# Optimization experiments

Hardware: AMD Instinct MI355X
Metric: run time of the kernel (lower is better)

## Reference

```python
import jax, jax.numpy as jnp
import numpy as np

H = 16  # n_heads

def setup_inputs() -> dict:
    key = jax.random.key(0)
    ks = jax.random.split(key, 11)
    B, L, D = 2, 2048, 1024
    w = 1.0 / np.sqrt(D).astype(np.float32)
    return {
        "query": jax.random.normal(ks[0], (B, L, D), jnp.float32),
        "key":   jax.random.normal(ks[1], (B, L, D), jnp.float32),
        "value": jax.random.normal(ks[2], (B, L, D), jnp.float32),
        "Wq": jax.random.normal(ks[3], (D, D), jnp.float32) * w,
        "bq": jax.random.normal(ks[4], (D,), jnp.float32) * 0.01,
        "Wk": jax.random.normal(ks[5], (D, D), jnp.float32) * w,
        "bk": jax.random.normal(ks[6], (D,), jnp.float32) * 0.01,
        "Wv": jax.random.normal(ks[7], (D, D), jnp.float32) * w,
        "bv": jax.random.normal(ks[8], (D,), jnp.float32) * 0.01,
        "Wo": jax.random.normal(ks[9], (D, D), jnp.float32) * w,
        "bo": jax.random.normal(ks[10], (D,), jnp.float32) * 0.01,
        "masksize": 256,
    }

def reference(query, key, value, Wq, bq, Wk, bk, Wv, bv, Wo, bo, masksize):
    B, L, D = query.shape
    d_k = D // H
    scale = 1.0 / np.sqrt(d_k).astype(np.float32)

    def proj(x, W, b):
        # nn.Linear: x @ W.T + b, then [B,L,H,d_k] -> [B,H,L,d_k]
        return (x @ W.T + b).reshape(B, L, H, d_k).transpose(0, 2, 1, 3)

    q = proj(query, Wq, bq)
    k = proj(key, Wk, bk)
    v = proj(value, Wv, bv)

    # Sliding-window float mask (faithful to original: a 0/1 FLOAT tensor is
    # passed as attn_mask to SDPA, so it is ADDED to scores, not -inf-masked).
    half = masksize // 2
    i = jnp.arange(L)[:, None]
    j = jnp.arange(L)[None, :]
    band = (jnp.abs(i - j) <= half).astype(q.dtype)  # [L, L]

    scores = jnp.einsum('bhqd,bhkd->bhqk', q, k) * scale + band  # [B,H,L,L]
    attn = jax.nn.softmax(scores, axis=-1)
    out = jnp.einsum('bhqk,bhkd->bhqd', attn, v)  # [B,H,L,d_k]
    out = out.transpose(0, 2, 1, 3).reshape(B, L, D)
    return out @ Wo.T + bo
```

## Files before the change

### kernel.cpp

```cpp
#include <hip/hip_runtime.h>
#include <hip/hip_bf16.h>

#define Hh 16
#define Ll 2048
#define Dd 1024
#define DK 64
#define Mm 4096
#define Kk 1024
#define Nn 1024

typedef short bf16x8 __attribute__((ext_vector_type(8)));
typedef float f32x4 __attribute__((ext_vector_type(4)));

static __device__ __forceinline__ unsigned short f2bf(float f) {
    union { __hip_bfloat16 b; unsigned short u; } cv;
    cv.b = __float2bfloat16(f);
    return cv.u;
}

static __device__ __forceinline__ unsigned packtr(float a, float b) {
    return __builtin_amdgcn_perm(__builtin_bit_cast(unsigned, b),
                                 __builtin_bit_cast(unsigned, a), 0x07060302u);
}

static __device__ __forceinline__ float fexp2(float x) {
    return __builtin_amdgcn_exp2f(x);
}

static __device__ __forceinline__ void glds16(const ushort* g, ushort* l) {
    __builtin_amdgcn_global_load_lds((const __attribute__((address_space(1))) unsigned int*)g,
                                     (__attribute__((address_space(3))) unsigned int*)l,
                                     16, 0, 0);
}

__global__ __launch_bounds__(256) void cast_all(
    const float* __restrict__ q, const float* __restrict__ k, const float* __restrict__ v,
    const float* __restrict__ wq, const float* __restrict__ wk, const float* __restrict__ wv,
    const float* __restrict__ wo,
    ushort* __restrict__ qb, ushort* __restrict__ kb, ushort* __restrict__ vb,
    ushort* __restrict__ wqb, ushort* __restrict__ wkb, ushort* __restrict__ wvb,
    ushort* __restrict__ wob) {
    const int bx = blockIdx.x;
    const float4* s; ushort4* d; int base;
    if      (bx <  4096) { s = (const float4*)q;  d = (ushort4*)qb;  base = 0; }
    else if (bx <  8192) { s = (const float4*)k;  d = (ushort4*)kb;  base = 4096; }
    else if (bx < 12288) { s = (const float4*)v;  d = (ushort4*)vb;  base = 8192; }
    else if (bx < 13312) { s = (const float4*)wq; d = (ushort4*)wqb; base = 12288; }
    else if (bx < 14336) { s = (const float4*)wk; d = (ushort4*)wkb; base = 13312; }
    else if (bx < 15360) { s = (const float4*)wv; d = (ushort4*)wvb; base = 14336; }
    else                 { s = (const float4*)wo; d = (ushort4*)wob; base = 15360; }
    const int i = (bx - base) * 256 + threadIdx.x;
    float4 vv = s[i];
    ushort4 o;
    o.x = f2bf(vv.x); o.y = f2bf(vv.y); o.z = f2bf(vv.z); o.w = f2bf(vv.w);
    d[i] = o;
}

__global__ __launch_bounds__(256) void gemm_qkv(
    const ushort* __restrict__ A0, const ushort* __restrict__ A1, const ushort* __restrict__ A2,
    const ushort* __restrict__ W0, const ushort* __restrict__ W1, const ushort* __restrict__ W2,
    const float* __restrict__ b0, const float* __restrict__ b1, const float* __restrict__ b2,
    ushort* __restrict__ O0, ushort* __restrict__ O1, ushort* __restrict__ OVt) {
    __shared__ __align__(16) ushort SM[2 * 16384];

    const int fl = blockIdx.x;
    const int xcd = fl & 7, bcoli = (fl >> 3) & 7, slot = fl >> 6;
    const int g = slot * 8 + xcd;
    const int z = g >> 5;
    const int browi = g & 31;

    const ushort* A = (z == 0) ? A0 : (z == 1) ? A1 : A2;
    const ushort* W = (z == 0) ? W0 : (z == 1) ? W1 : W2;
    const float* bias = (z == 0) ? b0 : (z == 1) ? b1 : b2;

    const int t = threadIdx.x;
    const int wave = t >> 6, lane = t & 63;
    const int quad = lane >> 4, l15 = lane & 15;
    const int brow = browi * 128, bcol = bcoli * 128;
    const int wr = (wave >> 1) * 64, wc = (wave & 1) * 64;
    const int sr = lane >> 3;
    const int sg = ((lane & 7) ^ sr) * 8;

    f32x4 acc[4][4] = {};

#define QSTAGE(K0, BUF)                                                                    \
    do {                                                                                   \
        ushort* As_ = SM + (BUF) * 16384;                                                  \
        ushort* Bs_ = SM + (BUF) * 16384 + 8192;                                           \
        _Pragma("unroll")                                                                  \
        for (int c_ = 0; c_ < 4; c_++) {                                                   \
            const int row_ = wave * 32 + c_ * 8;                                           \
            glds16(A + (size_t)(brow + row_ + sr) * Kk + (K0) + sg, As_ + row_ * 64);      \
            glds16(W + (size_t)(bcol + row_ + sr) * Kk + (K0) + sg, Bs_ + row_ * 64);      \
        }                                                                                  \
    } while (0)

    QSTAGE(0, 0);
    int cur = 0;

    for (int k0 = 0; k0 < Kk; k0 += 64) {
        __syncthreads();
        if (k0 + 64 < Kk) QSTAGE(k0 + 64, cur ^ 1);

        const ushort* As = SM + cur * 16384;
        const ushort* Bs = SM + cur * 16384 + 8192;

        bf16x8 af[2][4], bfr[2][4];
#pragma unroll
        for (int kk = 0; kk < 2; kk++) {
            const int pos8 = (((kk * 4 + quad) ^ (l15 & 7)) * 8);
#pragma unroll
            for (int i = 0; i < 4; i++)
                af[kk][i] = *(const bf16x8*)(As + (wr + i * 16 + l15) * 64 + pos8);
#pragma unroll
            for (int j = 0; j < 4; j++)
                bfr[kk][j] = *(const bf16x8*)(Bs + (wc + j * 16 + l15) * 64 + pos8);
        }
#pragma unroll
        for (int kk = 0; kk < 2; kk++)
#pragma unroll
            for (int i = 0; i < 4; i++)
#pragma unroll
                for (int j = 0; j < 4; j++)
                    acc[i][j] = __builtin_amdgcn_mfma_f32_16x16x32_bf16(af[kk][i], bfr[kk][j], acc[i][j], 0, 0, 0);
        cur ^= 1;
    }
#undef QSTAGE

    if (z < 2) {
        ushort* Out = (z == 0) ? O0 : O1;
        const float oscl = (z == 0) ? 0.18033688f : 1.0f;
        const int b = brow >> 11;
        const int lbase = (brow & 2047) + wr;
        const int h = (bcol + wc) >> 6;
        ushort* T = SM + wave * 1280;
        __syncthreads();
#pragma unroll
        for (int i = 0; i < 4; i++) {
#pragma unroll
            for (int j = 0; j < 4; j++) {
                const float bv = bias[bcol + wc + j * 16 + l15];
#pragma unroll
                for (int r = 0; r < 4; r++)
                    T[(quad * 4 + r) * 80 + j * 16 + l15] = f2bf((acc[i][j][r] + bv) * oscl);
            }
            const int r8 = lane >> 3, c8 = lane & 7;
#pragma unroll
            for (int pass = 0; pass < 2; pass++) {
                const uint4 val = *(const uint4*)(T + (pass * 8 + r8) * 80 + c8 * 8);
                const int l = lbase + i * 16 + pass * 8 + r8;
                *(uint4*)(Out + ((size_t)(b * Hh + h) * Ll + l) * DK + c8 * 8) = val;
            }
        }
    } else {
        ushort* T = SM;
        const int b = brow >> 11;
        const int lbase = brow & 2047;
        const int npr = (wave & 1) * 16 + l15;
#pragma unroll
        for (int j = 0; j < 4; j++) {
            __syncthreads();
            const float bv = bias[bcol + wc + j * 16 + l15];
#pragma unroll
            for (int i = 0; i < 4; i++)
#pragma unroll
                for (int r = 0; r < 4; r++) {
                    const int m = wr + i * 16 + quad * 4 + r;
                    T[npr * 136 + m] = f2bf(acc[i][j][r] + bv);
                }
            __syncthreads();
#pragma unroll
            for (int cc = 0; cc < 2; cc++) {
                const int idx = t + cc * 256;
                const int ni = idx >> 4;
                const int ms = idx & 15;
                const int n = bcol + (ni >> 4) * 64 + j * 16 + (ni & 15);
                const int hh = n >> 6, dk = n & 63;
                uint4 val = *(const uint4*)(T + ni * 136 + ms * 8);
                *(uint4*)(OVt + ((size_t)(b * Hh + hh) * DK + dk) * Ll + lbase + ms * 8) = val;
            }
        }
    }
}

__global__ __launch_bounds__(256, 2) void attn_kernel(const ushort* __restrict__ Q,
                                                      const ushort* __restrict__ Kp,
                                                      const ushort* __restrict__ Vt,
                                                      ushort* __restrict__ Oout,
                                                      const int* __restrict__ masksize) {
    __shared__ __align__(16) ushort SM[32768];
    const int t = threadIdx.x;
    const int wave = t >> 6, lane = t & 63;
    const int quad = lane >> 4, l15 = lane & 15;
    const int bx = blockIdx.x;
    const int bh = bx & 31, qc = bx >> 5;
    const int q0w = qc * 128 + wave * 32;
    const int half = masksize[0] >> 1;
    const unsigned wid = (unsigned)(2 * half);

    const ushort* Qb = Q + (size_t)bh * (Ll * DK);
    const ushort* Kb = Kp + (size_t)bh * (Ll * DK);
    const ushort* Vb = Vt + (size_t)bh * (DK * Ll);

    const bf16x8 qA0 = *(const bf16x8*)(Qb + (size_t)(q0w + l15) * DK + quad * 8);
    const bf16x8 qA1 = *(const bf16x8*)(Qb + (size_t)(q0w + l15) * DK + 32 + quad * 8);
    const bf16x8 qB0 = *(const bf16x8*)(Qb + (size_t)(q0w + 16 + l15) * DK + quad * 8);
    const bf16x8 qB1 = *(const bf16x8*)(Qb + (size_t)(q0w + 16 + l15) * DK + 32 + quad * 8);

    const float C2IN  = (1.0f - 24.0f) * 1.44269504088896f;
    const float C2OUT = -24.0f * 1.44269504088896f;
    const float E1 = 2.718281828f;

    bf16x8 onesf;
#pragma unroll
    for (int j = 0; j < 8; j++) onesf[j] = (short)0x3F80;

    f32x4 OA0[4] = {}, OB0[4] = {}, OA1[4] = {}, OB1[4] = {};
    f32x4 SA0 = {}, SB0 = {}, SA1 = {}, SB1 = {};

    const int krow = lane >> 2;
    const int kcol8 = (((lane & 3) ^ ((lane >> 3) & 3)) * 8);
    const int qsw8 = (quad ^ ((l15 >> 1) & 3)) * 8;
    const int vd8 = lane >> 3;
    const int vgp = 2 * (lane & 7);

#define STAGE_J(J, BUF)                                                                    \
    do {                                                                                   \
        const int kt0_ = (J) * 64, kt1_ = 1024 + (J) * 64;                                 \
        if (wave < 2) {                                                                    \
            const int ktk_ = (wave == 0) ? kt0_ : kt1_;                                    \
            ushort* dst_ = SM + wave * 8192 + (BUF) * 4096;                                \
            _Pragma("unroll")                                                              \
            for (int c_ = 0; c_ < 4; c_++)                                                 \
                _Pragma("unroll")                                                          \
                for (int pan_ = 0; pan_ < 2; pan_++)                                       \
                    glds16(Kb + (size_t)(ktk_ + c_ * 16 + krow) * DK + pan_ * 32 + kcol8,  \
                           dst_ + pan_ * 2048 + c_ * 512);                                 \
        } else {                                                                           \
            const int ktv_ = (wave == 2) ? kt0_ : kt1_;                                    \
            ushort* dst_ = SM + 16384 + (wave - 2) * 8192 + (BUF) * 4096;                  \
            _Pragma("unroll")                                                              \
            for (int s_ = 0; s_ < 8; s_++) {                                               \
                const int d_ = s_ * 8 + vd8;                                               \
                glds16(Vb + (size_t)d_ * Ll + ktv_ + ((vgp ^ (d_ & 14)) * 4),              \
                       dst_ + s_ * 512);                                                   \
            }                                                                              \
        }                                                                                  \
    } while (0)

#define STREAM_BODY(KB, VB, KT, CV, OAx, OBx, SAx, SBx, UNIF)                              \
    _Pragma("unroll")                                                                      \
    for (int s = 0; s < 2; s++) {                                                          \
        const bf16x8 kf00 = *(const bf16x8*)((KB) + ((2 * s) * 16 + l15) * 32 + qsw8);     \
        const bf16x8 kf01 = *(const bf16x8*)((KB) + 2048 + ((2 * s) * 16 + l15) * 32 + qsw8); \
        const bf16x8 kf10 = *(const bf16x8*)((KB) + ((2 * s + 1) * 16 + l15) * 32 + qsw8); \
        const bf16x8 kf11 = *(const bf16x8*)((KB) + 2048 + ((2 * s + 1) * 16 + l15) * 32 + qsw8); \
        f32x4 zA0 = __builtin_amdgcn_mfma_f32_16x16x32_bf16(kf00, qA0, (CV), 0, 0, 0);     \
        zA0 = __builtin_amdgcn_mfma_f32_16x16x32_bf16(kf01, qA1, zA0, 0, 0, 0);            \
        f32x4 zA1 = __builtin_amdgcn_mfma_f32_16x16x32_bf16(kf10, qA0, (CV), 0, 0, 0);     \
        zA1 = __builtin_amdgcn_mfma_f32_16x16x32_bf16(kf11, qA1, zA1, 0, 0, 0);            \
        f32x4 zB0 = __builtin_amdgcn_mfma_f32_16x16x32_bf16(kf00, qB0, (CV), 0, 0, 0);     \
        zB0 = __builtin_amdgcn_mfma_f32_16x16x32_bf16(kf01, qB1, zB0, 0, 0, 0);            \
        f32x4 zB1 = __builtin_amdgcn_mfma_f32_16x16x32_bf16(kf10, qB0, (CV), 0, 0, 0);     \
        zB1 = __builtin_amdgcn_mfma_f32_16x16x32_bf16(kf11, qB1, zB1, 0, 0, 0);            \
        float pA[8], pB[8];                                                                \
        if (UNIF) {                                                                        \
            _Pragma("unroll")                                                              \
            for (int g = 0; g < 2; g++)                                                    \
                _Pragma("unroll")                                                          \
                for (int r = 0; r < 4; r++) {                                              \
                    pA[g * 4 + r] = fexp2(g ? zA1[r] : zA0[r]);                            \
                    pB[g * 4 + r] = fexp2(g ? zB1[r] : zB0[r]);                            \
                }                                                                          \
        } else {                                                                           \
            const int kb = (KT) + s * 32 + quad * 4 + half;                                \
            _Pragma("unroll")                                                              \
            for (int g = 0; g < 2; g++)                                                    \
                _Pragma("unroll")                                                          \
                for (int r = 0; r < 4; r++) {                                              \
                    const unsigned ttA = (unsigned)(kb + g * 16 + r - (q0w + l15));        \
                    const unsigned ttB = (unsigned)(kb + g * 16 + r - (q0w + 16 + l15));   \
                    pA[g * 4 + r] = fexp2(g ? zA1[r] : zA0[r]) * (ttA <= wid ? E1 : 1.0f); \
                    pB[g * 4 + r] = fexp2(g ? zB1[r] : zB0[r]) * (ttB <= wid ? E1 : 1.0f); \
                }                                                                          \
        }                                                                                  \
        bf16x8 pfA, pfB;                                                                   \
        ((unsigned*)&pfA)[0] = packtr(pA[0], pA[1]);                                       \
        ((unsigned*)&pfA)[1] = packtr(pA[2], pA[3]);                                       \
        ((unsigned*)&pfA)[2] = packtr(pA[4], pA[5]);                                       \
        ((unsigned*)&pfA)[3] = packtr(pA[6], pA[7]);                                       \
        ((unsigned*)&pfB)[0] = packtr(pB[0], pB[1]);                                       \
        ((unsigned*)&pfB)[1] = packtr(pB[2], pB[3]);                                       \
        ((unsigned*)&pfB)[2] = packtr(pB[4], pB[5]);                                       \
        ((unsigned*)&pfB)[3] = packtr(pB[6], pB[7]);                                       \
        SAx = __builtin_amdgcn_mfma_f32_16x16x32_bf16(pfA, onesf, SAx, 0, 0, 0);           \
        SBx = __builtin_amdgcn_mfma_f32_16x16x32_bf16(pfB, onesf, SBx, 0, 0, 0);           \
        _Pragma("unroll")                                                                  \
        for (int i = 0; i < 4; i++) {                                                      \
            const int bi = (i * 16 + l15) * 64;                                            \
            const int x14 = l15 & 14;                                                      \
            const ushort4 v1 = *(const ushort4*)((VB) + bi + (((s * 8 + quad) ^ x14) * 4)); \
            const ushort4 v2 = *(const ushort4*)((VB) + bi + (((s * 8 + 4 + quad) ^ x14) * 4)); \
            bf16x8 vc;                                                                     \
            *(ushort4*)&vc = v1;                                                           \
            *((ushort4*)&vc + 1) = v2;                                                     \
            OAx[i] = __builtin_amdgcn_mfma_f32_16x16x32_bf16(pfA, vc, OAx[i], 0, 0, 0);    \
            OBx[i] = __builtin_amdgcn_mfma_f32_16x16x32_bf16(pfB, vc, OBx[i], 0, 0, 0);    \
        }                                                                                  \
    }

    STAGE_J(0, 0);
    int cur = 0;
    const int qlo = q0w, qhi = q0w + 31;

    for (int j = 0; j < 16; ++j) {
        const int kt0 = j * 64, kt1 = 1024 + j * 64;
        __syncthreads();
        if (j < 15) STAGE_J(j + 1, cur ^ 1);

        const ushort* K0b = SM + cur * 4096;
        const ushort* K1b = SM + 8192 + cur * 4096;
        const ushort* V0b = SM + 16384 + cur * 4096;
        const ushort* V1b = SM + 24576 + cur * 4096;

        const bool allout0 = (kt0 + 63 < qlo - half) || (kt0 > qhi + half);
        const bool allin0  = (kt0 >= qhi - half) && (kt0 + 63 <= qlo + half);
        const bool allout1 = (kt1 + 63 < qlo - half) || (kt1 > qhi + half);
        const bool allin1  = (kt1 >= qhi - half) && (kt1 + 63 <= qlo + half);

        if ((allin0 || allout0) && (allin1 || allout1)) {
            const float c0 = allin0 ? C2IN : C2OUT;
            const float c1 = allin1 ? C2IN : C2OUT;
            const f32x4 cv0 = {c0, c0, c0, c0};
            const f32x4 cv1 = {c1, c1, c1, c1};
            STREAM_BODY(K0b, V0b, kt0, cv0, OA0, OB0, SA0, SB0, 1);
            STREAM_BODY(K1b, V1b, kt1, cv1, OA1, OB1, SA1, SB1, 1);
        } else {
            const f32x4 cvo = {C2OUT, C2OUT, C2OUT, C2OUT};
            STREAM_BODY(K0b, V0b, kt0, cvo, OA0, OB0, SA0, SB0, 0);
            STREAM_BODY(K1b, V1b, kt1, cvo, OA1, OB1, SA1, SB1, 0);
        }
        cur ^= 1;
    }
#undef STAGE_J
#undef STREAM_BODY

    float liA[4], liB[4];
#pragma unroll
    for (int r = 0; r < 4; r++) {
        liA[r] = 1.0f / (SA0[r] + SA1[r]);
        liB[r] = 1.0f / (SB0[r] + SB1[r]);
    }

    const int b = bh >> 4, h = bh & 15;
#pragma unroll
    for (int i = 0; i < 4; i++)
#pragma unroll
        for (int r = 0; r < 4; r++) {
            const int qa = q0w + quad * 4 + r;
            Oout[((size_t)b * Ll + qa) * Dd + h * DK + i * 16 + l15] =
                f2bf((OA0[i][r] + OA1[i][r]) * liA[r]);
            Oout[((size_t)b * Ll + qa + 16) * Dd + h * DK + i * 16 + l15] =
                f2bf((OB0[i][r] + OB1[i][r]) * liB[r]);
        }
}

__global__ __launch_bounds__(256) void gemm_o(const ushort* __restrict__ A,
                                              const ushort* __restrict__ W,
                                              const float* __restrict__ bias,
                                              float* __restrict__ Out) {
    __shared__ __align__(16) ushort SM[2 * 16384];
    const int fl = blockIdx.x;
    const int xcd = fl & 7, bcoli = (fl >> 3) & 7, slot = fl >> 6;
    const int browi = slot * 8 + xcd;
    const int t = threadIdx.x;
    const int wave = t >> 6, lane = t & 63;
    const int quad = lane >> 4, l15 = lane & 15;
    const int brow = browi * 128, bcol = bcoli * 128;
    const int wr = (wave >> 1) * 64, wc = (wave & 1) * 64;
    const int sr = lane >> 3;
    const int sg = ((lane & 7) ^ sr) * 8;

    f32x4 acc[4][4] = {};

#define OSTAGE(K0, BUF)                                                                    \
    do {                                                                                   \
        ushort* As_ = SM + (BUF) * 16384;                                                  \
        ushort* Bs_ = SM + (BUF) * 16384 + 8192;                                           \
        _Pragma("unroll")                                                                  \
        for (int c_ = 0; c_ < 4; c_++) {                                                   \
            const int row_ = wave * 32 + c_ * 8;                                           \
            glds16(A + (size_t)(brow + row_ + sr) * Kk + (K0) + sg, As_ + row_ * 64);      \
            glds16(W + (size_t)(bcol + row_ + sr) * Kk + (K0) + sg, Bs_ + row_ * 64);      \
        }                                                                                  \
    } while (0)

    OSTAGE(0, 0);
    int cur = 0;

    for (int k0 = 0; k0 < Kk; k0 += 64) {
        __syncthreads();
        if (k0 + 64 < Kk) OSTAGE(k0 + 64, cur ^ 1);

        const ushort* As = SM + cur * 16384;
        const ushort* Bs = SM + cur * 16384 + 8192;

        bf16x8 af[2][4], bfr[2][4];
#pragma unroll
        for (int kk = 0; kk < 2; kk++) {
            const int pos8 = (((kk * 4 + quad) ^ (l15 & 7)) * 8);
#pragma unroll
            for (int i = 0; i < 4; i++)
                af[kk][i] = *(const bf16x8*)(As + (wr + i * 16 + l15) * 64 + pos8);
#pragma unroll
            for (int j = 0; j < 4; j++)
                bfr[kk][j] = *(const bf16x8*)(Bs + (wc + j * 16 + l15) * 64 + pos8);
        }
#pragma unroll
        for (int kk = 0; kk < 2; kk++)
#pragma unroll
            for (int i = 0; i < 4; i++)
#pragma unroll
                for (int j = 0; j < 4; j++)
                    acc[i][j] = __builtin_amdgcn_mfma_f32_16x16x32_bf16(af[kk][i], bfr[kk][j], acc[i][j], 0, 0, 0);
        cur ^= 1;
    }
#undef OSTAGE

#pragma unroll
    for (int i = 0; i < 4; i++)
#pragma unroll
        for (int j = 0; j < 4; j++) {
            const int n = bcol + wc + j * 16 + l15;
            const float bv = bias[n];
#pragma unroll
            for (int r = 0; r < 4; r++) {
                const int m = brow + wr + i * 16 + quad * 4 + r;
                Out[(size_t)m * Nn + n] = acc[i][j][r] + bv;
            }
        }
}

extern "C" void kernel_launch(void* const* d_in, const int* in_sizes, int n_in,
                              void* d_out, int out_size, void* d_ws, size_t ws_size,
                              hipStream_t stream) {
    const float* query = (const float*)d_in[0];
    const float* key   = (const float*)d_in[1];
    const float* value = (const float*)d_in[2];
    const float* Wq = (const float*)d_in[3];
    const float* bq = (const float*)d_in[4];
    const float* Wk = (const float*)d_in[5];
    const float* bk = (const float*)d_in[6];
    const float* Wv = (const float*)d_in[7];
    const float* bv = (const float*)d_in[8];
    const float* Wo = (const float*)d_in[9];
    const float* bo = (const float*)d_in[10];
    const int* masksize = (const int*)d_in[11];

    char* ws = (char*)d_ws;
    const size_t MB = 1024 * 1024;
    ushort* qb  = (ushort*)(ws + 0 * MB);
    ushort* kbf = (ushort*)(ws + 8 * MB);
    ushort* vbf = (ushort*)(ws + 16 * MB);
    ushort* wqb = (ushort*)(ws + 24 * MB);
    ushort* wkb = (ushort*)(ws + 26 * MB);
    ushort* wvb = (ushort*)(ws + 28 * MB);
    ushort* wob = (ushort*)(ws + 30 * MB);
    ushort* Qp  = (ushort*)(ws + 32 * MB);
    ushort* Kp  = (ushort*)(ws + 40 * MB);
    ushort* Vt  = (ushort*)(ws + 48 * MB);
    ushort* AO  = (ushort*)(ws + 56 * MB);

    cast_all<<<16384, 256, 0, stream>>>(query, key, value, Wq, Wk, Wv, Wo,
                                        qb, kbf, vbf, wqb, wkb, wvb, wob);

    gemm_qkv<<<768, 256, 0, stream>>>(qb, kbf, vbf,
                                      wqb, wkb, wvb,
                                      bq, bk, bv,
                                      Qp, Kp, Vt);

    attn_kernel<<<512, 256, 0, stream>>>(Qp, Kp, Vt, AO, masksize);

    gemm_o<<<256, 256, 0, stream>>>(AO, wob, bo, (float*)d_out);
}
```

Measured before the change: 206.9 us.

## Fuse fp32-to-bf16 activation cast into QKV GEMM operand loading

```diff
diff --git a/kernel.cpp b/kernel.cpp
--- a/kernel.cpp
+++ b/kernel.cpp
@@ -33,22 +33,17 @@
                                      16, 0, 0);
 }
 
-__global__ __launch_bounds__(256) void cast_all(
-    const float* __restrict__ q, const float* __restrict__ k, const float* __restrict__ v,
+__global__ __launch_bounds__(256) void cast_w(
     const float* __restrict__ wq, const float* __restrict__ wk, const float* __restrict__ wv,
     const float* __restrict__ wo,
-    ushort* __restrict__ qb, ushort* __restrict__ kb, ushort* __restrict__ vb,
     ushort* __restrict__ wqb, ushort* __restrict__ wkb, ushort* __restrict__ wvb,
     ushort* __restrict__ wob) {
     const int bx = blockIdx.x;
     const float4* s; ushort4* d; int base;
-    if      (bx <  4096) { s = (const float4*)q;  d = (ushort4*)qb;  base = 0; }
-    else if (bx <  8192) { s = (const float4*)k;  d = (ushort4*)kb;  base = 4096; }
-    else if (bx < 12288) { s = (const float4*)v;  d = (ushort4*)vb;  base = 8192; }
-    else if (bx < 13312) { s = (const float4*)wq; d = (ushort4*)wqb; base = 12288; }
-    else if (bx < 14336) { s = (const float4*)wk; d = (ushort4*)wkb; base = 13312; }
-    else if (bx < 15360) { s = (const float4*)wv; d = (ushort4*)wvb; base = 14336; }
-    else                 { s = (const float4*)wo; d = (ushort4*)wob; base = 15360; }
+    if      (bx < 1024) { s = (const float4*)wq; d = (ushort4*)wqb; base = 0; }
+    else if (bx < 2048) { s = (const float4*)wk; d = (ushort4*)wkb; base = 1024; }
+    else if (bx < 3072) { s = (const float4*)wv; d = (ushort4*)wvb; base = 2048; }
+    else                { s = (const float4*)wo; d = (ushort4*)wob; base = 3072; }
     const int i = (bx - base) * 256 + threadIdx.x;
     float4 vv = s[i];
     ushort4 o;
@@ -57,7 +52,7 @@
 }
 
 __global__ __launch_bounds__(256) void gemm_qkv(
-    const ushort* __restrict__ A0, const ushort* __restrict__ A1, const ushort* __restrict__ A2,
+    const float* __restrict__ A0, const float* __restrict__ A1, const float* __restrict__ A2,
     const ushort* __restrict__ W0, const ushort* __restrict__ W1, const ushort* __restrict__ W2,
     const float* __restrict__ b0, const float* __restrict__ b1, const float* __restrict__ b2,
     ushort* __restrict__ O0, ushort* __restrict__ O1, ushort* __restrict__ OVt) {
@@ -69,7 +64,7 @@
     const int z = g >> 5;
     const int browi = g & 31;
 
-    const ushort* A = (z == 0) ? A0 : (z == 1) ? A1 : A2;
+    const float* Aact = (z == 0) ? A0 : (z == 1) ? A1 : A2;
     const ushort* W = (z == 0) ? W0 : (z == 1) ? W1 : W2;
     const float* bias = (z == 0) ? b0 : (z == 1) ? b1 : b2;
 
@@ -79,28 +74,52 @@
     const int brow = browi * 128, bcol = bcoli * 128;
     const int wr = (wave >> 1) * 64, wc = (wave & 1) * 64;
     const int sr = lane >> 3;
+    const int ag = (lane & 7) * 8;
     const int sg = ((lane & 7) ^ sr) * 8;
+    const int awg = ((lane & 7) ^ sr) * 8;
 
     f32x4 acc[4][4] = {};
-
-#define QSTAGE(K0, BUF)                                                                    \
+    float4 rA[4][2];
+
+#define QISSUE(K0, BUF)                                                                    \
     do {                                                                                   \
-        ushort* As_ = SM + (BUF) * 16384;                                                  \
         ushort* Bs_ = SM + (BUF) * 16384 + 8192;                                           \
         _Pragma("unroll")                                                                  \
         for (int c_ = 0; c_ < 4; c_++) {                                                   \
             const int row_ = wave * 32 + c_ * 8;                                           \
-            glds16(A + (size_t)(brow + row_ + sr) * Kk + (K0) + sg, As_ + row_ * 64);      \
+            const float* asrc_ = Aact + (size_t)(brow + row_ + sr) * Kk + (K0) + ag;       \
+            rA[c_][0] = *(const float4*)asrc_;                                             \
+            rA[c_][1] = *(const float4*)(asrc_ + 4);                                       \
             glds16(W + (size_t)(bcol + row_ + sr) * Kk + (K0) + sg, Bs_ + row_ * 64);      \
         }                                                                                  \
     } while (0)
 
-    QSTAGE(0, 0);
+#define QWRITE(BUF)                                                                        \
+    do {                                                                                   \
+        ushort* As_ = SM + (BUF) * 16384;                                                  \
+        _Pragma("unroll")                                                                  \
+        for (int c_ = 0; c_ < 4; c_++) {                                                   \
+            const int row_ = wave * 32 + c_ * 8;                                           \
+            bf16x8 v_;                                                                     \
+            v_[0] = (short)f2bf(rA[c_][0].x);                                              \
+            v_[1] = (short)f2bf(rA[c_][0].y);                                              \
+            v_[2] = (short)f2bf(rA[c_][0].z);                                              \
+            v_[3] = (short)f2bf(rA[c_][0].w);                                              \
+            v_[4] = (short)f2bf(rA[c_][1].x);                                              \
+            v_[5] = (short)f2bf(rA[c_][1].y);                                              \
+            v_[6] = (short)f2bf(rA[c_][1].z);                                              \
+            v_[7] = (short)f2bf(rA[c_][1].w);                                              \
+            *(bf16x8*)(As_ + (row_ + sr) * 64 + awg) = v_;                                 \
+        }                                                                                  \
+    } while (0)
+
+    QISSUE(0, 0);
+    QWRITE(0);
     int cur = 0;
 
     for (int k0 = 0; k0 < Kk; k0 += 64) {
         __syncthreads();
-        if (k0 + 64 < Kk) QSTAGE(k0 + 64, cur ^ 1);
+        if (k0 + 64 < Kk) QISSUE(k0 + 64, cur ^ 1);
 
         const ushort* As = SM + cur * 16384;
         const ushort* Bs = SM + cur * 16384 + 8192;
@@ -123,9 +142,12 @@
 #pragma unroll
                 for (int j = 0; j < 4; j++)
                     acc[i][j] = __builtin_amdgcn_mfma_f32_16x16x32_bf16(af[kk][i], bfr[kk][j], acc[i][j], 0, 0, 0);
+
+        if (k0 + 64 < Kk) QWRITE(cur ^ 1);
         cur ^= 1;
     }
-#undef QSTAGE
+#undef QISSUE
+#undef QWRITE
 
     if (z < 2) {
         ushort* Out = (z == 0) ? O0 : O1;
@@ -459,9 +481,6 @@
 
     char* ws = (char*)d_ws;
     const size_t MB = 1024 * 1024;
-    ushort* qb  = (ushort*)(ws + 0 * MB);
-    ushort* kbf = (ushort*)(ws + 8 * MB);
-    ushort* vbf = (ushort*)(ws + 16 * MB);
     ushort* wqb = (ushort*)(ws + 24 * MB);
     ushort* wkb = (ushort*)(ws + 26 * MB);
     ushort* wvb = (ushort*)(ws + 28 * MB);
@@ -471,10 +490,9 @@
     ushort* Vt  = (ushort*)(ws + 48 * MB);
     ushort* AO  = (ushort*)(ws + 56 * MB);
 
-    cast_all<<<16384, 256, 0, stream>>>(query, key, value, Wq, Wk, Wv, Wo,
-                                        qb, kbf, vbf, wqb, wkb, wvb, wob);
-
-    gemm_qkv<<<768, 256, 0, stream>>>(qb, kbf, vbf,
+    cast_w<<<4096, 256, 0, stream>>>(Wq, Wk, Wv, Wo, wqb, wkb, wvb, wob);
+
+    gemm_qkv<<<768, 256, 0, stream>>>(query, key, value,
                                       wqb, wkb, wvb,
                                       bq, bk, bv,
                                       Qp, Kp, Vt);
```

New measurement: 221.6 us. 7.1% more time.
